# Kernel tuning notes

Hardware: AMD Instinct MI355X
Metric: run time of the kernel (lower is better)

Reference implementation:

```python
import jax, jax.numpy as jnp
import numpy as np

D_MODEL = 1024
N_HEADS = 16
D_HEAD = D_MODEL // N_HEADS


def setup_inputs() -> dict:
    key = jax.random.key(0)
    ks = jax.random.split(key, 11)
    B, L = 2, 2048
    s = 1.0 / np.sqrt(D_MODEL)
    return {
        "query": jax.random.normal(ks[0], (B, L, D_MODEL), jnp.float32),
        "key": jax.random.normal(ks[1], (B, L, D_MODEL), jnp.float32),
        "value": jax.random.normal(ks[2], (B, L, D_MODEL), jnp.float32),
        "Wq": jax.random.normal(ks[3], (D_MODEL, D_MODEL), jnp.float32) * s,
        "bq": jnp.zeros((D_MODEL,), jnp.float32),
        "Wk": jax.random.normal(ks[4], (D_MODEL, D_MODEL), jnp.float32) * s,
        "bk": jnp.zeros((D_MODEL,), jnp.float32),
        "Wv": jax.random.normal(ks[5], (D_MODEL, D_MODEL), jnp.float32) * s,
        "bv": jnp.zeros((D_MODEL,), jnp.float32),
        "Wo": jax.random.normal(ks[6], (D_MODEL, D_MODEL), jnp.float32) * s,
        "bo": jnp.zeros((D_MODEL,), jnp.float32),
    }


def reference(query, key, value, Wq, bq, Wk, bk, Wv, bv, Wo, bo):
    B, Lq, _ = query.shape
    Lk = key.shape[1]
    scale = D_HEAD ** -0.5
    # projections; weights stored as [in, out] (torch Linear applies x @ W.T; here W is already transposed)
    q = (query @ Wq + bq).reshape(B, Lq, N_HEADS, D_HEAD).transpose(0, 2, 1, 3)  # [B,H,Lq,dh]
    k = (key @ Wk + bk).reshape(B, Lk, N_HEADS, D_HEAD).transpose(0, 2, 1, 3)
    v = (value @ Wv + bv).reshape(B, Lk, N_HEADS, D_HEAD).transpose(0, 2, 1, 3)
    scores = jnp.einsum('bhqd,bhkd->bhqk', q, k) * scale  # [B,H,Lq,Lk]
    # causal mask (is_causal=True)
    causal = jnp.triu(jnp.ones((Lq, Lk), dtype=bool), k=1)
    scores = jnp.where(causal, -jnp.inf, scores)
    attn = jax.nn.softmax(scores, axis=-1)
    out = jnp.einsum('bhqk,bhkd->bhqd', attn, v)  # [B,H,Lq,dh]
    out = out.transpose(0, 2, 1, 3).reshape(B, Lq, D_MODEL)
    return out @ Wo + bo
```

## Files before the change

### kernel.cpp

```cpp
#include <hip/hip_runtime.h>
#include <hip/hip_bf16.h>

typedef __bf16 bf16x8 __attribute__((ext_vector_type(8)));
typedef __bf16 bf16x4 __attribute__((ext_vector_type(4)));
typedef float floatx4 __attribute__((ext_vector_type(4)));

#define MFMA16(a, b, c) __builtin_amdgcn_mfma_f32_16x16x32_bf16(a, b, c, 0, 0, 0)
#define AS1 __attribute__((address_space(1)))
#define AS3 __attribute__((address_space(3)))

constexpr int D = 1024;
constexpr int L = 2048;
constexpr int BB = 2;
constexpr int DH = 64;
constexpr float NEG_BIG = -1e30f;
constexpr float SCALE_LOG2E = 0.125f * 1.4426950408889634f;

__device__ __forceinline__ void gld16(const __bf16* g, __bf16* l) {
  __builtin_amdgcn_global_load_lds((AS1 void*)g, (AS3 void*)l, 16, 0, 0);
}

__global__ __launch_bounds__(256) void cvt_x(const float* __restrict__ xq, const float* __restrict__ xk,
                                             const float* __restrict__ xv, __bf16* __restrict__ out) {
  const int z = blockIdx.z;
  const float* src = z == 0 ? xq : z == 1 ? xk : xv;
  __bf16* dst = out + (size_t)z * BB * L * D;
  const int N = BB * L * D;
  const int stride = gridDim.x * 256 * 4;
  for (int i = (blockIdx.x * 256 + threadIdx.x) * 4; i < N; i += stride) {
    float4 f = *(const float4*)&src[i];
    bf16x4 b = {(__bf16)f.x, (__bf16)f.y, (__bf16)f.z, (__bf16)f.w};
    *(bf16x4*)&dst[i] = b;
  }
}

__global__ void transpose_w(const float* __restrict__ w0, const float* __restrict__ w1,
                            const float* __restrict__ w2, const float* __restrict__ w3,
                            __bf16* __restrict__ out) {
  __shared__ __bf16 tile[32][33];
  int mat = blockIdx.z;
  const float* src = mat == 0 ? w0 : mat == 1 ? w1 : mat == 2 ? w2 : w3;
  __bf16* dst = out + (size_t)mat * D * D;
  int bx = blockIdx.x * 32, by = blockIdx.y * 32;
  int tx = threadIdx.x, ty = threadIdx.y;
#pragma unroll
  for (int i = 0; i < 32; i += 8)
    tile[ty + i][tx] = (__bf16)src[(size_t)(by + ty + i) * D + bx + tx];
  __syncthreads();
#pragma unroll
  for (int i = 0; i < 32; i += 8)
    dst[(size_t)(bx + ty + i) * D + by + tx] = tile[tx][ty + i];
}

__device__ __forceinline__ void stage32(const __bf16* __restrict__ A, const __bf16* __restrict__ Bt,
                                        __bf16* sA, __bf16* sB, int m0, int n0, int kb,
                                        int r, int sc, int dst) {
  gld16(&A[(size_t)(m0 + r) * 1024 + kb + sc],       &sA[dst]);
  gld16(&A[(size_t)(m0 + 64 + r) * 1024 + kb + sc],  &sA[2048 + dst]);
  gld16(&Bt[(size_t)(n0 + r) * 1024 + kb + sc],      &sB[dst]);
  gld16(&Bt[(size_t)(n0 + 64 + r) * 1024 + kb + sc], &sB[2048 + dst]);
}

__device__ __forceinline__ void gemm_core(const __bf16* __restrict__ A, const __bf16* __restrict__ Bt,
                                          __bf16* sm, int m0, int n0, int wm, int wn,
                                          int l15, int quad, int t, floatx4 (&acc)[4][4]) {
  const int r = t >> 2;
  const int sc = ((t & 3) ^ ((r >> 1) & 3)) * 8;
  const int dst = t * 8;
  const int sw2 = (l15 >> 1) & 3;

  stage32(A, Bt, sm, sm + 8192, m0, n0, 0, r, sc, dst);

  int cur = 0;
  for (int kb = 0; kb < 1024; kb += 32) {
    if (kb + 32 < 1024) {
      stage32(A, Bt, sm + (cur ^ 1) * 4096, sm + 8192 + (cur ^ 1) * 4096, m0, n0, kb + 32, r, sc, dst);
      asm volatile("s_waitcnt vmcnt(4)" ::: "memory");
    } else {
      asm volatile("s_waitcnt vmcnt(0)" ::: "memory");
    }
    __builtin_amdgcn_s_barrier();

    const __bf16* sAc = sm + cur * 4096;
    const __bf16* sBc = sm + 8192 + cur * 4096;
    bf16x8 af[4], bf_[4];
#pragma unroll
    for (int i = 0; i < 4; i++) {
      const int row = wm * 64 + i * 16 + l15;
      af[i] = *(const bf16x8*)&sAc[(row * 4 + (quad ^ sw2)) * 8];
    }
#pragma unroll
    for (int j = 0; j < 4; j++) {
      const int row = wn * 64 + j * 16 + l15;
      bf_[j] = *(const bf16x8*)&sBc[(row * 4 + (quad ^ sw2)) * 8];
    }
    asm volatile("s_waitcnt lgkmcnt(0)" ::: "memory");
    __builtin_amdgcn_sched_barrier(0);
    __builtin_amdgcn_s_barrier();

#pragma unroll
    for (int i = 0; i < 4; i++)
#pragma unroll
      for (int j = 0; j < 4; j++)
        acc[i][j] = MFMA16(af[i], bf_[j], acc[i][j]);

    cur ^= 1;
  }
}

__global__ __launch_bounds__(256, 3) void gemm_proj(const __bf16* __restrict__ xc, const __bf16* __restrict__ wt,
                                                    const float* __restrict__ bq, const float* __restrict__ bk,
                                                    const float* __restrict__ bv, __bf16* __restrict__ qkv) {
  __shared__ __align__(16) __bf16 smem[17408];

  const int flat = (blockIdx.z * 32 + blockIdx.y) * 8 + blockIdx.x;
  const int s = (flat & 7) * 96 + (flat >> 3);
  const int z = s >> 8;
  const int rem = s & 255;
  const int by = rem >> 3, bx = rem & 7;

  const __bf16* A = xc + (size_t)z * BB * L * D;
  const __bf16* Bt = wt + (size_t)z * D * D;
  const float* bias = z == 0 ? bq : z == 1 ? bk : bv;
  __bf16* dst = qkv + (size_t)z * BB * L * D;

  const int t = threadIdx.x;
  const int lane = t & 63;
  const int w = t >> 6;
  const int wm = w >> 1, wn = w & 1;
  const int l15 = lane & 15, quad = lane >> 4;
  const int m0 = by * 128, n0 = bx * 128;

  floatx4 acc[4][4];
#pragma unroll
  for (int i = 0; i < 4; i++)
#pragma unroll
    for (int j = 0; j < 4; j++) acc[i][j] = (floatx4){0.f, 0.f, 0.f, 0.f};

  gemm_core(A, Bt, smem, m0, n0, wm, wn, l15, quad, t, acc);

  float bvv[4];
#pragma unroll
  for (int j = 0; j < 4; j++) bvv[j] = bias[n0 + wn * 64 + j * 16 + l15];

  constexpr int TP = 136;
  __bf16* T = smem;
  if (z < 2) {
#pragma unroll
    for (int i = 0; i < 4; i++) {
      const int mrowb = wm * 64 + i * 16 + quad * 4;
#pragma unroll
      for (int j = 0; j < 4; j++) {
        const int ccol = wn * 64 + j * 16 + l15;
#pragma unroll
        for (int rr = 0; rr < 4; rr++) {
          float val = acc[i][j][rr] + bvv[j];
          if (z == 0) val *= SCALE_LOG2E;
          T[(mrowb + rr) * TP + ccol] = (__bf16)val;
        }
      }
    }
  } else {
#pragma unroll
    for (int i = 0; i < 4; i++) {
      const int mrowb = wm * 64 + i * 16 + quad * 4;
#pragma unroll
      for (int j = 0; j < 4; j++) {
        const int ccol = wn * 64 + j * 16 + l15;
        bf16x4 v4;
#pragma unroll
        for (int rr = 0; rr < 4; rr++) v4[rr] = (__bf16)(acc[i][j][rr] + bvv[j]);
        *(bf16x4*)&T[ccol * TP + mrowb] = v4;
      }
    }
  }
  __syncthreads();

  const int b = m0 >> 11;
  const int l0 = m0 & 2047;
  if (z < 2) {
#pragma unroll
    for (int sH = 0; sH < 8; sH++) {
      const int c = sH * 256 + t;
      const int mrow = c >> 4, k16 = c & 15;
      const int h = (n0 >> 6) + (k16 >> 3);
      const int d0 = (k16 & 7) * 8;
      bf16x8 v = *(const bf16x8*)&T[mrow * TP + k16 * 8];
      *(bf16x8*)&dst[((size_t)(b * 16 + h) * 2048 + l0 + mrow) * 64 + d0] = v;
    }
  } else {
    const int R0 = (b * 16 + (n0 >> 6)) * 64;
#pragma unroll
    for (int sH = 0; sH < 8; sH++) {
      const int c = sH * 256 + t;
      const int ccol = c >> 4, k16 = c & 15;
      bf16x8 v = *(const bf16x8*)&T[ccol * TP + k16 * 8];
      *(bf16x8*)&dst[(size_t)(R0 + ccol) * 2048 + l0 + k16 * 8] = v;
    }
  }
}

__global__ __launch_bounds__(256, 3) void gemm_o(const __bf16* __restrict__ ctx, const __bf16* __restrict__ wto,
                                                 const float* __restrict__ bo, float* __restrict__ out) {
  __shared__ __align__(16) __bf16 smem[16384];

  const int flat = blockIdx.y * 8 + blockIdx.x;
  const int s = (flat & 7) * 32 + (flat >> 3);
  const int by = s >> 3, bx = s & 7;

  const int t = threadIdx.x;
  const int lane = t & 63;
  const int w = t >> 6;
  const int wm = w >> 1, wn = w & 1;
  const int l15 = lane & 15, quad = lane >> 4;
  const int m0 = by * 128, n0 = bx * 128;

  floatx4 acc[4][4];
#pragma unroll
  for (int i = 0; i < 4; i++)
#pragma unroll
    for (int j = 0; j < 4; j++) acc[i][j] = (floatx4){0.f, 0.f, 0.f, 0.f};

  gemm_core(ctx, wto, smem, m0, n0, wm, wn, l15, quad, t, acc);

  float bvv[4];
#pragma unroll
  for (int j = 0; j < 4; j++) bvv[j] = bo[n0 + wn * 64 + j * 16 + l15];

#pragma unroll
  for (int i = 0; i < 4; i++) {
    const int rowb = m0 + wm * 64 + i * 16 + quad * 4;
#pragma unroll
    for (int j = 0; j < 4; j++) {
      const int col = n0 + wn * 64 + j * 16 + l15;
#pragma unroll
      for (int rr = 0; rr < 4; rr++)
        out[(size_t)(rowb + rr) * 1024 + col] = acc[i][j][rr] + bvv[j];
    }
  }
}

__global__ __launch_bounds__(256, 4) void flash_attn(const __bf16* __restrict__ q, const __bf16* __restrict__ k,
                                                     const __bf16* __restrict__ vT, __bf16* __restrict__ ctx) {
  __shared__ __align__(16) __bf16 kbuf[2][4096];
  __shared__ __align__(16) __bf16 vbuf[2][4096];

  const int t = threadIdx.x;
  const int lane = t & 63;
  const int w = t >> 6;
  const int l15 = lane & 15, quad = lane >> 4;
  const int bh = blockIdx.y;
  const int p = (blockIdx.x + blockIdx.y) & 15;

  const __bf16* qb = q + (size_t)bh * L * DH;
  const __bf16* kb_ = k + (size_t)bh * L * DH;
  const __bf16* vb = vT + (size_t)bh * DH * L;

  const int c0 = t, c1 = 256 + t;
  const int kr0 = c0 >> 3, kd0 = ((c0 & 7) ^ (kr0 & 7)) * 8;
  const int kr1 = c1 >> 3, kd1 = ((c1 & 7) ^ (kr1 & 7)) * 8;

  const int b = bh >> 4, h = bh & 15;

#pragma unroll 1
  for (int pass = 0; pass < 2; ++pass) {
    const int qt = pass == 0 ? p : 31 - p;
    const int q0 = qt * 64;
    const int qg = q0 + w * 16;
    const int qrow = qg + l15;
    bf16x8 aq0 = *(const bf16x8*)&qb[(size_t)qrow * 64 + quad * 8];
    bf16x8 aq1 = *(const bf16x8*)&qb[(size_t)qrow * 64 + 32 + quad * 8];

    floatx4 o[4];
#pragma unroll
    for (int nt = 0; nt < 4; nt++) o[nt] = (floatx4){0.f, 0.f, 0.f, 0.f};
    float psum = 0.f;

    gld16(&kb_[(size_t)kr0 * 64 + kd0], &kbuf[0][c0 * 8]);
    gld16(&kb_[(size_t)kr1 * 64 + kd1], &kbuf[0][c1 * 8]);
    gld16(&vb[(size_t)kr0 * L + kd0],   &vbuf[0][c0 * 8]);
    gld16(&vb[(size_t)kr1 * L + kd1],   &vbuf[0][c1 * 8]);
    __syncthreads();

    for (int it = 0; it <= qt; ++it) {
      const int cur = it & 1;
      const int kt = it * 64;

      if (it < qt) {
        const int ktn = kt + 64;
        gld16(&kb_[(size_t)(ktn + kr0) * 64 + kd0], &kbuf[cur ^ 1][c0 * 8]);
        gld16(&kb_[(size_t)(ktn + kr1) * 64 + kd1], &kbuf[cur ^ 1][c1 * 8]);
        gld16(&vb[(size_t)kr0 * L + ktn + kd0],     &vbuf[cur ^ 1][c0 * 8]);
        gld16(&vb[(size_t)kr1 * L + ktn + kd1],     &vbuf[cur ^ 1][c1 * 8]);
      }

      const bool diag = (it == qt);

#pragma unroll
      for (int sp = 0; sp < 2; ++sp) {
        floatx4 z[2];
#pragma unroll
        for (int u = 0; u < 2; ++u) {
          const int kr = (2 * sp + u) * 16 + l15;
          bf16x8 kf0 = *(const bf16x8*)&kbuf[cur][(kr * 8 + (quad ^ (kr & 7))) * 8];
          bf16x8 kf1 = *(const bf16x8*)&kbuf[cur][(kr * 8 + ((quad + 4) ^ (kr & 7))) * 8];
          floatx4 zz = (floatx4){0.f, 0.f, 0.f, 0.f};
          zz = MFMA16(kf0, aq0, zz);
          zz = MFMA16(kf1, aq1, zz);
          z[u] = zz;
        }

        if (diag) {
#pragma unroll
          for (int u = 0; u < 2; ++u) {
            const int kgb = kt + (2 * sp + u) * 16 + quad * 4;
#pragma unroll
            for (int rr = 0; rr < 4; rr++)
              if (kgb + rr > qrow) z[u][rr] = NEG_BIG;
          }
        }

        bf16x8 pa;
#pragma unroll
        for (int u = 0; u < 2; ++u)
#pragma unroll
          for (int rr = 0; rr < 4; rr++) {
            const float pv = __builtin_amdgcn_exp2f(z[u][rr]);
            psum += pv;
            pa[u * 4 + rr] = (__bf16)pv;
          }

#pragma unroll
        for (int nt = 0; nt < 4; nt++) {
          const int d = nt * 16 + l15;
          const int x0 = (sp * 4 + (quad >> 1)) ^ (d & 7);
          const int x1 = (sp * 4 + 2 + (quad >> 1)) ^ (d & 7);
          union { bf16x8 v8; bf16x4 v4[2]; } uv;
          uv.v4[0] = *(const bf16x4*)&vbuf[cur][(d * 8 + x0) * 8 + (quad & 1) * 4];
          uv.v4[1] = *(const bf16x4*)&vbuf[cur][(d * 8 + x1) * 8 + (quad & 1) * 4];
          o[nt] = MFMA16(pa, uv.v8, o[nt]);
        }
      }
      __syncthreads();
    }

    psum += __shfl_xor(psum, 16);
    psum += __shfl_xor(psum, 32);
    const float invs = 1.f / psum;

#pragma unroll
    for (int rr = 0; rr < 4; rr++) {
      const float inv = __shfl(invs, (lane & 48) + quad * 4 + rr);
      const int row = qg + quad * 4 + rr;
#pragma unroll
      for (int nt = 0; nt < 4; nt++) {
        const int col = h * 64 + nt * 16 + l15;
        ctx[((size_t)b * L + row) * 1024 + col] = (__bf16)(o[nt][rr] * inv);
      }
    }
  }
}

extern "C" void kernel_launch(void* const* d_in, const int* in_sizes, int n_in,
                              void* d_out, int out_size, void* d_ws, size_t ws_size,
                              hipStream_t stream) {
  const float* x_q = (const float*)d_in[0];
  const float* x_k = (const float*)d_in[1];
  const float* x_v = (const float*)d_in[2];
  const float* Wq  = (const float*)d_in[3];
  const float* bq  = (const float*)d_in[4];
  const float* Wk  = (const float*)d_in[5];
  const float* bk  = (const float*)d_in[6];
  const float* Wv  = (const float*)d_in[7];
  const float* bv  = (const float*)d_in[8];
  const float* Wo  = (const float*)d_in[9];
  const float* bo  = (const float*)d_in[10];

  char* ws = (char*)d_ws;
  __bf16* xc  = (__bf16*)ws;
  __bf16* wt  = (__bf16*)(ws + ((size_t)24 << 20));
  __bf16* qkv = (__bf16*)(ws + ((size_t)32 << 20));
  __bf16* ctx = (__bf16*)ws;
  __bf16* qp  = qkv;
  __bf16* kp  = qkv + (size_t)BB * L * D;
  __bf16* vtp = qkv + (size_t)2 * BB * L * D;

  cvt_x<<<dim3(1024, 1, 3), 256, 0, stream>>>(x_q, x_k, x_v, xc);
  transpose_w<<<dim3(32, 32, 4), dim3(32, 8), 0, stream>>>(Wq, Wk, Wv, Wo, wt);
  gemm_proj<<<dim3(8, 32, 3), 256, 0, stream>>>(xc, wt, bq, bk, bv, qkv);
  flash_attn<<<dim3(16, 32), 256, 0, stream>>>(qp, kp, vtp, ctx);
  gemm_o<<<dim3(8, 32), 256, 0, stream>>>(ctx, wt + (size_t)3 * D * D, bo, (float*)d_out);
}
```

Before: 209.9 us.

## Process both causal query tiles in one pass sharing K/V tiles

```diff
diff --git a/kernel.cpp b/kernel.cpp
--- a/kernel.cpp
+++ b/kernel.cpp
@@ -240,7 +240,7 @@
   }
 }
 
-__global__ __launch_bounds__(256, 4) void flash_attn(const __bf16* __restrict__ q, const __bf16* __restrict__ k,
+__global__ __launch_bounds__(256, 2) void flash_attn(const __bf16* __restrict__ q, const __bf16* __restrict__ k,
                                                      const __bf16* __restrict__ vT, __bf16* __restrict__ ctx) {
   __shared__ __align__(16) __bf16 kbuf[2][4096];
   __shared__ __align__(16) __bf16 vbuf[2][4096];
@@ -251,6 +251,8 @@
   const int l15 = lane & 15, quad = lane >> 4;
   const int bh = blockIdx.y;
   const int p = (blockIdx.x + blockIdx.y) & 15;
+  const int qtA = 31 - p;
+  const int qtB = p;
 
   const __bf16* qb = q + (size_t)bh * L * DH;
   const __bf16* kb_ = k + (size_t)bh * L * DH;
@@ -260,103 +262,144 @@
   const int kr0 = c0 >> 3, kd0 = ((c0 & 7) ^ (kr0 & 7)) * 8;
   const int kr1 = c1 >> 3, kd1 = ((c1 & 7) ^ (kr1 & 7)) * 8;
 
-  const int b = bh >> 4, h = bh & 15;
+  const int qrA = qtA * 64 + w * 16 + l15;
+  const int qrB = qtB * 64 + w * 16 + l15;
+  const bf16x8 aqA0 = *(const bf16x8*)&qb[(size_t)qrA * 64 + quad * 8];
+  const bf16x8 aqA1 = *(const bf16x8*)&qb[(size_t)qrA * 64 + 32 + quad * 8];
+  const bf16x8 aqB0 = *(const bf16x8*)&qb[(size_t)qrB * 64 + quad * 8];
+  const bf16x8 aqB1 = *(const bf16x8*)&qb[(size_t)qrB * 64 + 32 + quad * 8];
+
+  floatx4 oA[4], oB[4];
+#pragma unroll
+  for (int nt = 0; nt < 4; nt++) {
+    oA[nt] = (floatx4){0.f, 0.f, 0.f, 0.f};
+    oB[nt] = (floatx4){0.f, 0.f, 0.f, 0.f};
+  }
+  float psA = 0.f, psB = 0.f;
+
+  gld16(&kb_[(size_t)kr0 * 64 + kd0], &kbuf[0][c0 * 8]);
+  gld16(&kb_[(size_t)kr1 * 64 + kd1], &kbuf[0][c1 * 8]);
+  gld16(&vb[(size_t)kr0 * L + kd0],   &vbuf[0][c0 * 8]);
+  gld16(&vb[(size_t)kr1 * L + kd1],   &vbuf[0][c1 * 8]);
 
 #pragma unroll 1
-  for (int pass = 0; pass < 2; ++pass) {
-    const int qt = pass == 0 ? p : 31 - p;
-    const int q0 = qt * 64;
-    const int qg = q0 + w * 16;
-    const int qrow = qg + l15;
-    bf16x8 aq0 = *(const bf16x8*)&qb[(size_t)qrow * 64 + quad * 8];
-    bf16x8 aq1 = *(const bf16x8*)&qb[(size_t)qrow * 64 + 32 + quad * 8];
-
-    floatx4 o[4];
-#pragma unroll
-    for (int nt = 0; nt < 4; nt++) o[nt] = (floatx4){0.f, 0.f, 0.f, 0.f};
-    float psum = 0.f;
-
-    gld16(&kb_[(size_t)kr0 * 64 + kd0], &kbuf[0][c0 * 8]);
-    gld16(&kb_[(size_t)kr1 * 64 + kd1], &kbuf[0][c1 * 8]);
-    gld16(&vb[(size_t)kr0 * L + kd0],   &vbuf[0][c0 * 8]);
-    gld16(&vb[(size_t)kr1 * L + kd1],   &vbuf[0][c1 * 8]);
-    __syncthreads();
-
-    for (int it = 0; it <= qt; ++it) {
-      const int cur = it & 1;
-      const int kt = it * 64;
-
-      if (it < qt) {
-        const int ktn = kt + 64;
-        gld16(&kb_[(size_t)(ktn + kr0) * 64 + kd0], &kbuf[cur ^ 1][c0 * 8]);
-        gld16(&kb_[(size_t)(ktn + kr1) * 64 + kd1], &kbuf[cur ^ 1][c1 * 8]);
-        gld16(&vb[(size_t)kr0 * L + ktn + kd0],     &vbuf[cur ^ 1][c0 * 8]);
-        gld16(&vb[(size_t)kr1 * L + ktn + kd1],     &vbuf[cur ^ 1][c1 * 8]);
-      }
-
-      const bool diag = (it == qt);
-
-#pragma unroll
-      for (int sp = 0; sp < 2; ++sp) {
-        floatx4 z[2];
+  for (int it = 0; it <= qtA; ++it) {
+    const int cur = it & 1;
+    const int kt = it * 64;
+
+    if (it < qtA) {
+      const int ktn = kt + 64;
+      gld16(&kb_[(size_t)(ktn + kr0) * 64 + kd0], &kbuf[cur ^ 1][c0 * 8]);
+      gld16(&kb_[(size_t)(ktn + kr1) * 64 + kd1], &kbuf[cur ^ 1][c1 * 8]);
+      gld16(&vb[(size_t)kr0 * L + ktn + kd0],     &vbuf[cur ^ 1][c0 * 8]);
+      gld16(&vb[(size_t)kr1 * L + ktn + kd1],     &vbuf[cur ^ 1][c1 * 8]);
+      asm volatile("s_waitcnt vmcnt(4)" ::: "memory");
+    } else {
+      asm volatile("s_waitcnt vmcnt(0)" ::: "memory");
+    }
+    __builtin_amdgcn_s_barrier();
+
+    const bool diagA = (it == qtA);
+    const bool doB   = (it <= qtB);
+    const bool diagB = (it == qtB);
+
+#pragma unroll
+    for (int sp = 0; sp < 2; ++sp) {
+      bf16x8 kf0[2], kf1[2];
+#pragma unroll
+      for (int u = 0; u < 2; ++u) {
+        const int kr = (2 * sp + u) * 16 + l15;
+        kf0[u] = *(const bf16x8*)&kbuf[cur][(kr * 8 + (quad ^ (kr & 7))) * 8];
+        kf1[u] = *(const bf16x8*)&kbuf[cur][(kr * 8 + ((quad + 4) ^ (kr & 7))) * 8];
+      }
+
+      bf16x8 paA;
+#pragma unroll
+      for (int u = 0; u < 2; ++u) {
+        floatx4 zz = (floatx4){0.f, 0.f, 0.f, 0.f};
+        zz = MFMA16(kf0[u], aqA0, zz);
+        zz = MFMA16(kf1[u], aqA1, zz);
+        if (diagA) {
+          const int kgb = kt + (2 * sp + u) * 16 + quad * 4;
+#pragma unroll
+          for (int rr = 0; rr < 4; rr++)
+            if (kgb + rr > qrA) zz[rr] = NEG_BIG;
+        }
+#pragma unroll
+        for (int rr = 0; rr < 4; rr++) {
+          const float pv = __builtin_amdgcn_exp2f(zz[rr]);
+          psA += pv;
+          paA[u * 4 + rr] = (__bf16)pv;
+        }
+      }
+
+      bf16x8 paB;
+      if (doB) {
 #pragma unroll
         for (int u = 0; u < 2; ++u) {
-          const int kr = (2 * sp + u) * 16 + l15;
-          bf16x8 kf0 = *(const bf16x8*)&kbuf[cur][(kr * 8 + (quad ^ (kr & 7))) * 8];
-          bf16x8 kf1 = *(const bf16x8*)&kbuf[cur][(kr * 8 + ((quad + 4) ^ (kr & 7))) * 8];
           floatx4 zz = (floatx4){0.f, 0.f, 0.f, 0.f};
-          zz = MFMA16(kf0, aq0, zz);
-          zz = MFMA16(kf1, aq1, zz);
-          z[u] = zz;
-        }
-
-        if (diag) {
-#pragma unroll
-          for (int u = 0; u < 2; ++u) {
+          zz = MFMA16(kf0[u], aqB0, zz);
+          zz = MFMA16(kf1[u], aqB1, zz);
+          if (diagB) {
             const int kgb = kt + (2 * sp + u) * 16 + quad * 4;
 #pragma unroll
             for (int rr = 0; rr < 4; rr++)
-              if (kgb + rr > qrow) z[u][rr] = NEG_BIG;
+              if (kgb + rr > qrB) zz[rr] = NEG_BIG;
+          }
+#pragma unroll
+          for (int rr = 0; rr < 4; rr++) {
+            const float pv = __builtin_amdgcn_exp2f(zz[rr]);
+            psB += pv;
+            paB[u * 4 + rr] = (__bf16)pv;
           }
         }
-
-        bf16x8 pa;
-#pragma unroll
-        for (int u = 0; u < 2; ++u)
-#pragma unroll
-          for (int rr = 0; rr < 4; rr++) {
-            const float pv = __builtin_amdgcn_exp2f(z[u][rr]);
-            psum += pv;
-            pa[u * 4 + rr] = (__bf16)pv;
-          }
-
-#pragma unroll
-        for (int nt = 0; nt < 4; nt++) {
-          const int d = nt * 16 + l15;
-          const int x0 = (sp * 4 + (quad >> 1)) ^ (d & 7);
-          const int x1 = (sp * 4 + 2 + (quad >> 1)) ^ (d & 7);
-          union { bf16x8 v8; bf16x4 v4[2]; } uv;
-          uv.v4[0] = *(const bf16x4*)&vbuf[cur][(d * 8 + x0) * 8 + (quad & 1) * 4];
-          uv.v4[1] = *(const bf16x4*)&vbuf[cur][(d * 8 + x1) * 8 + (quad & 1) * 4];
-          o[nt] = MFMA16(pa, uv.v8, o[nt]);
-        }
-      }
-      __syncthreads();
-    }
-
-    psum += __shfl_xor(psum, 16);
-    psum += __shfl_xor(psum, 32);
-    const float invs = 1.f / psum;
-
-#pragma unroll
-    for (int rr = 0; rr < 4; rr++) {
-      const float inv = __shfl(invs, (lane & 48) + quad * 4 + rr);
-      const int row = qg + quad * 4 + rr;
+      }
+
 #pragma unroll
       for (int nt = 0; nt < 4; nt++) {
-        const int col = h * 64 + nt * 16 + l15;
-        ctx[((size_t)b * L + row) * 1024 + col] = (__bf16)(o[nt][rr] * inv);
-      }
+        const int d = nt * 16 + l15;
+        const int x0 = (sp * 4 + (quad >> 1)) ^ (d & 7);
+        const int x1 = (sp * 4 + 2 + (quad >> 1)) ^ (d & 7);
+        union { bf16x8 v8; bf16x4 v4[2]; } uv;
+        uv.v4[0] = *(const bf16x4*)&vbuf[cur][(d * 8 + x0) * 8 + (quad & 1) * 4];
+        uv.v4[1] = *(const bf16x4*)&vbuf[cur][(d * 8 + x1) * 8 + (quad & 1) * 4];
+        oA[nt] = MFMA16(paA, uv.v8, oA[nt]);
+        if (doB) oB[nt] = MFMA16(paB, uv.v8, oB[nt]);
+      }
+    }
+
+    asm volatile("s_waitcnt lgkmcnt(0)" ::: "memory");
+    __builtin_amdgcn_sched_barrier(0);
+    __builtin_amdgcn_s_barrier();
+  }
+
+  const int b = bh >> 4, h = bh & 15;
+
+  psA += __shfl_xor(psA, 16);
+  psA += __shfl_xor(psA, 32);
+  const float invA = 1.f / psA;
+#pragma unroll
+  for (int rr = 0; rr < 4; rr++) {
+    const float inv = __shfl(invA, (lane & 48) + quad * 4 + rr);
+    const int row = qtA * 64 + w * 16 + quad * 4 + rr;
+#pragma unroll
+    for (int nt = 0; nt < 4; nt++) {
+      const int col = h * 64 + nt * 16 + l15;
+      ctx[((size_t)b * L + row) * 1024 + col] = (__bf16)(oA[nt][rr] * inv);
+    }
+  }
+
+  psB += __shfl_xor(psB, 16);
+  psB += __shfl_xor(psB, 32);
+  const float invB = 1.f / psB;
+#pragma unroll
+  for (int rr = 0; rr < 4; rr++) {
+    const float inv = __shfl(invB, (lane & 48) + quad * 4 + rr);
+    const int row = qtB * 64 + w * 16 + quad * 4 + rr;
+#pragma unroll
+    for (int nt = 0; nt < 4; nt++) {
+      const int col = h * 64 + nt * 16 + l15;
+      ctx[((size_t)b * L + row) * 1024 + col] = (__bf16)(oB[nt][rr] * inv);
     }
   }
 }
```

Measured after the change: 213.5 us. Within noise of the previous version (+1.7%).
